# Optimization experiments

Hardware: AMD Instinct MI355X
Metric: run time of the kernel (lower is better)

The kernel has to match this reference:

```python
import jax, jax.numpy as jnp
import numpy as np

N_NODES = 20000
N_EDGES = 320000
N_GRAPHS = 64
SEQ = 20
SCALAR = 16
EMB = 32
HID = 128
HEADS = 4
IN_DIM = SCALAR + 5 * EMB  # 176
NEG_SLOPE = 0.2


def masked_mean_embed(table, idx):
    # table: [V, EMB], idx: [N, L] with 0 = padding
    emb = table[idx]                                  # [N, L, EMB]
    mask = (idx != 0).astype(emb.dtype)[..., None]    # [N, L, 1]
    return (emb * mask).sum(axis=1) / (mask.sum(axis=1) + 1e-9)


def gat_conv(x, src, dst, W, att_src, att_dst, bias, heads, out_ch):
    # PyG GATConv (add_self_loops already applied to src/dst), concat heads.
    N = x.shape[0]
    xw = (x @ W).reshape(N, heads, out_ch)            # [N, H, C]
    a_src = (xw * att_src).sum(-1)                    # [N, H]
    a_dst = (xw * att_dst).sum(-1)                    # [N, H]
    e = jax.nn.leaky_relu(a_src[src] + a_dst[dst], NEG_SLOPE)  # [E, H]
    e_max = jax.ops.segment_max(e, dst, num_segments=N)
    e_max = jnp.where(jnp.isfinite(e_max), e_max, 0.0)
    ex = jnp.exp(e - e_max[dst])                      # [E, H]
    denom = jax.ops.segment_sum(ex, dst, num_segments=N)
    alpha = ex / (denom[dst] + 1e-16)                 # [E, H]
    msg = xw[src] * alpha[:, :, None]                 # [E, H, C]
    out = jax.ops.segment_sum(msg, dst, num_segments=N)
    return out.reshape(N, heads * out_ch) + bias


def setup_inputs() -> dict:
    key = jax.random.key(0)
    ks = jax.random.split(key, 24)
    s = 0.05
    inp = {
        "x_scalar": jax.random.normal(ks[0], (N_NODES, SCALAR), jnp.float32),
        "x_opcode": jax.random.randint(ks[1], (N_NODES, SEQ), 0, 256),
        "x_source": jax.random.randint(ks[2], (N_NODES, SEQ), 0, 512),
        "x_sink": jax.random.randint(ks[3], (N_NODES, SEQ), 0, 512),
        "x_string_manip": jax.random.randint(ks[4], (N_NODES, SEQ), 0, 128),
        "x_payload": jax.random.randint(ks[5], (N_NODES, SEQ), 0, 1024),
        "edge_index": jax.random.randint(ks[6], (2, N_EDGES), 0, N_NODES),
        "batch": jnp.sort(jax.random.randint(ks[7], (N_NODES,), 0, N_GRAPHS)),
        # embedding tables (row 0 = padding; masked out anyway)
        "emb_opcode": jax.random.normal(ks[8], (256, EMB)) * s,
        "emb_source": jax.random.normal(ks[9], (512, EMB)) * s,
        "emb_sink": jax.random.normal(ks[10], (512, EMB)) * s,
        "emb_string": jax.random.normal(ks[11], (128, EMB)) * s,
        "emb_payload": jax.random.normal(ks[12], (1024, EMB)) * s,
        "ln_gamma": jnp.ones((IN_DIM,), jnp.float32),
        "ln_beta": jnp.zeros((IN_DIM,), jnp.float32),
        "W1": jax.random.normal(ks[13], (IN_DIM, HEADS * HID)) * s,
        "att_src1": jax.random.normal(ks[14], (HEADS, HID)) * s,
        "att_dst1": jax.random.normal(ks[15], (HEADS, HID)) * s,
        "b1": jnp.zeros((HEADS * HID,), jnp.float32),
        "W2": jax.random.normal(ks[16], (HEADS * HID, HID)) * s,
        "att_src2": jax.random.normal(ks[17], (1, HID)) * s,
        "att_dst2": jax.random.normal(ks[18], (1, HID)) * s,
        "b2": jnp.zeros((HID,), jnp.float32),
        "cls_w1": jax.random.normal(ks[19], (HID, HID // 2)) * s,
        "cls_b1": jnp.zeros((HID // 2,), jnp.float32),
        "cls_w2": jax.random.normal(ks[20], (HID // 2, 2)) * s,
        "cls_b2": jnp.zeros((2,), jnp.float32),
    }
    return inp


def reference(x_scalar, x_opcode, x_source, x_sink, x_string_manip, x_payload,
              edge_index, batch,
              emb_opcode, emb_source, emb_sink, emb_string, emb_payload,
              ln_gamma, ln_beta,
              W1, att_src1, att_dst1, b1,
              W2, att_src2, att_dst2, b2,
              cls_w1, cls_b1, cls_w2, cls_b2):
    feats = jnp.concatenate([
        x_scalar,
        masked_mean_embed(emb_opcode, x_opcode),
        masked_mean_embed(emb_source, x_source),
        masked_mean_embed(emb_sink, x_sink),
        masked_mean_embed(emb_string, x_string_manip),
        masked_mean_embed(emb_payload, x_payload),
    ], axis=1)  # [N, 176]
    mu = feats.mean(-1, keepdims=True)
    var = ((feats - mu) ** 2).mean(-1, keepdims=True)
    h = (feats - mu) / jnp.sqrt(var + 1e-5) * ln_gamma + ln_beta

    # add self loops (PyG GATConv default)
    loops = jnp.arange(N_NODES, dtype=edge_index.dtype)
    src = jnp.concatenate([edge_index[0], loops])
    dst = jnp.concatenate([edge_index[1], loops])

    x = jax.nn.elu(gat_conv(h, src, dst, W1, att_src1, att_dst1, b1, HEADS, HID))
    x = jax.nn.elu(gat_conv(x, src, dst, W2, att_src2, att_dst2, b2, 1, HID))

    pooled = jax.ops.segment_max(x, batch, num_segments=N_GRAPHS)  # [G, HID]
    hcls = jax.nn.relu(pooled @ cls_w1 + cls_b1)
    return hcls @ cls_w2 + cls_b2  # [G, 2]
```

## Files before the change

### kernel.cpp

```cpp
#include <hip/hip_runtime.h>
#include <hip/hip_bf16.h>
#include <math.h>

#define N_NODES 20000
#define N_EDGES 320000
#define N_GRAPHS 64
#define SEQ 20
#define SCALAR 16
#define EMB 32
#define HID 128
#define IN_DIM 176
#define TOT_EDGES (N_EDGES + N_NODES)
#define CHUNK_SMALL 10000
#define POOL_SLICES 32

typedef _Float16 half8v __attribute__((ext_vector_type(8)));
typedef float f32x4 __attribute__((ext_vector_type(4)));
#define LO_SCALE 2048.0f
#define LO_INV (1.0f / 2048.0f)

#define PB2_ELEMS (16 * 8 * 64 * 8)
#define PB1_ELEMS (4 * 6 * 8 * 64 * 8)

#define SETUP_BLOCKS 124
#define COUNT_BLOCKS ((TOT_EDGES + 255) / 256)
#define NB4 ((N_NODES + 3) / 4)

__device__ inline float readlane_f(float v, int l) {
  return __uint_as_float(__builtin_amdgcn_readlane(__float_as_uint(v), l));
}
__device__ inline int readlane_i(int v, int l) {
  return __builtin_amdgcn_readlane(v, l);
}
__device__ inline float leaky(float e) { return e >= 0.f ? e : 0.2f * e; }
__device__ inline float elu(float v) { return v > 0.f ? v : expf(v) - 1.f; }

__global__ __launch_bounds__(256) void setup_count_kernel(
    const float* __restrict__ W1, const float* __restrict__ att_s1,
    const float* __restrict__ att_d1, const float* __restrict__ W2,
    const int* __restrict__ edge_index, const int* __restrict__ batch,
    float* __restrict__ was4, float* __restrict__ wad4,
    _Float16* __restrict__ PB1h, _Float16* __restrict__ PB1l,
    _Float16* __restrict__ PB2h, _Float16* __restrict__ PB2l,
    int* __restrict__ cnt, int* __restrict__ gstarts) {
  int b = blockIdx.x;
  if (b < 44) {
    int lane = threadIdx.x & 63;
    int k = b * 4 + (threadIdx.x >> 6);
    if (k >= IN_DIM) return;
    const float* wrow = W1 + (size_t)k * 512;
    float s[4], d[4];
#pragma unroll
    for (int hh = 0; hh < 4; ++hh) {
      float w0 = wrow[hh * 128 + lane], w1 = wrow[hh * 128 + 64 + lane];
      float a0 = att_s1[hh * 128 + lane], a1 = att_s1[hh * 128 + 64 + lane];
      float c0 = att_d1[hh * 128 + lane], c1 = att_d1[hh * 128 + 64 + lane];
      s[hh] = w0 * a0 + w1 * a1;
      d[hh] = w0 * c0 + w1 * c1;
    }
    for (int off = 1; off < 64; off <<= 1) {
#pragma unroll
      for (int hh = 0; hh < 4; ++hh) {
        s[hh] += __shfl_xor(s[hh], off);
        d[hh] += __shfl_xor(d[hh], off);
      }
    }
    if (lane == 0) {
      *(float4*)&was4[k * 4] = make_float4(s[0], s[1], s[2], s[3]);
      *(float4*)&wad4[k * 4] = make_float4(d[0], d[1], d[2], d[3]);
    }
  } else if (b < 92) {
    int t = (b - 44) * 256 + threadIdx.x;
    int lane = t & 63, wi = t >> 6;
    int r = lane & 15, g = lane >> 4;
    int ntile = wi & 7, rem = wi >> 3;
    int ks = rem % 6, hh = rem / 6;
    int col = hh * 128 + ntile * 16 + r;
    size_t o = ((size_t)wi * 64 + lane) * 8;
#pragma unroll
// ... 10 lines not shown
    int r = lane & 15, g = lane >> 4;
    int ks = wi >> 3, ntile = wi & 7;
    int col = ntile * 16 + r;
    size_t o = ((size_t)wi * 64 + lane) * 8;
#pragma unroll
    for (int j = 0; j < 8; ++j) {
      int k = ks * 32 + g * 8 + j;
      float v = W2[(size_t)k * 128 + col];
      _Float16 h = (_Float16)v;
      PB2h[o + j] = h;
      PB2l[o + j] = (_Float16)((v - (float)h) * LO_SCALE);
    }
  } else if (b < SETUP_BLOCKS + COUNT_BLOCKS) {
    int i = (b - SETUP_BLOCKS) * 256 + threadIdx.x;
    if (i < N_EDGES) {
      atomicAdd(&cnt[edge_index[N_EDGES + i]], 1);
    } else if (i < TOT_EDGES) {
      atomicAdd(&cnt[i - N_EDGES], 1);
    }
  } else {
    int t = threadIdx.x;
    if (t > N_GRAPHS) return;
    int lo = 0, hi = N_NODES;
    while (lo < hi) {
      int mid = (lo + hi) >> 1;
      if (batch[mid] < t) lo = mid + 1; else hi = mid;
    }
    gstarts[t] = lo;
  }
}

__global__ __launch_bounds__(1024) void prefix_kernel(const int* __restrict__ cnt,
                                                      int* __restrict__ indptr,
                                                      int n, int total) {
  __shared__ int ss[1024];
  int t = threadIdx.x;
  int per = (n + 1023) / 1024;
  int beg = t * per, end = min(beg + per, n);
  int s = 0;
  for (int i = beg; i < end; ++i) s += cnt[i];
  ss[t] = s;
  __syncthreads();
  for (int off = 1; off < 1024; off <<= 1) {
    int v = (t >= off) ? ss[t - off] : 0;
    __syncthreads();
    ss[t] += v;
    __syncthreads();
  }
  int run = ss[t] - s;
  for (int i = beg; i < end; ++i) { indptr[i] = run; run += cnt[i]; }
  if (t == 0) indptr[n] = total;
}

__global__ __launch_bounds__(256) void scatter_feats_kernel(
    const int* __restrict__ edge_index, const int* __restrict__ indptr,
    int* __restrict__ cursor, int* __restrict__ srcs,
    const float* __restrict__ xs,
    const int* __restrict__ i0, const int* __restrict__ i1,
    const int* __restrict__ i2, const int* __restrict__ i3,
    const int* __restrict__ i4,
    const float* __restrict__ t0, const float* __restrict__ t1,
    const float* __restrict__ t2, const float* __restrict__ t3,
    const float* __restrict__ t4,
    const float* __restrict__ gamma, const float* __restrict__ beta,
    const float* __restrict__ was4, const float* __restrict__ wad4,
    float* __restrict__ hout, float* __restrict__ a_s,
    float* __restrict__ a_d) {
  int b = blockIdx.x;
  if (b < COUNT_BLOCKS) {
    int i = b * 256 + threadIdx.x;
    int s, d;
    if (i < N_EDGES) { s = edge_index[i]; d = edge_index[N_EDGES + i]; }
    else if (i < TOT_EDGES) { s = i - N_EDGES; d = s; }
    else return;
    int pos = indptr[d] + atomicAdd(&cursor[d], 1);
    srcs[pos] = s;
    return;
  }
  int lane = threadIdx.x & 63;
  int w = threadIdx.x >> 6;
  int n = (b - COUNT_BLOCKS) * 4 + w;
  if (n >= N_NODES) return;
  __shared__ int sidx[4][100];
  {
    int j = lane;
    int tab = j / 20, l = j - tab * 20;
    const int* ip = tab == 0 ? i0 : tab == 1 ? i1 : tab == 2 ? i2 : i3;
    sidx[w][j] = ip[n * SEQ + l];
    if (lane < 36) {
      int j2 = 64 + lane;
      int tab2 = j2 / 20, l2 = j2 - tab2 * 20;
      const int* ip2 = tab2 == 3 ? i3 : i4;
      sidx[w][j2] = ip2[n * SEQ + l2];
    }
  }
  bool l48 = lane < 48;
  float f0, f1, f2 = 0.f;
  if (lane < SCALAR) {
    f0 = xs[n * SCALAR + lane];
  } else {
    int tt = lane - SCALAR, tab = tt >> 5, d = tt & 31;
    const float* tp = tab == 0 ? t0 : t1;
    float sum = 0.f, cnt = 0.f;
#pragma unroll
    for (int l = 0; l < SEQ; ++l) {
      int id = sidx[w][tab * 20 + l];
      if (id != 0) { sum += tp[id * EMB + d]; cnt += 1.f; }
    }
    f0 = sum / (cnt + 1e-9f);
  }
  {
    int tt = 48 + lane, tab = tt >> 5, d = tt & 31;
    const float* tp = tab == 1 ? t1 : tab == 2 ? t2 : t3;
    float sum = 0.f, cnt = 0.f;
#pragma unroll
    for (int l = 0; l < SEQ; ++l) {
      int id = sidx[w][tab * 20 + l];
      if (id != 0) { sum += tp[id * EMB + d]; cnt += 1.f; }
    }
    f1 = sum / (cnt + 1e-9f);
  }
  if (l48) {
    int tt = 112 + lane, tab = tt >> 5, d = tt & 31;
    const float* tp = tab == 3 ? t3 : t4;
    float sum = 0.f, cnt = 0.f;
#pragma unroll
    for (int l = 0; l < SEQ; ++l) {
      int id = sidx[w][tab * 20 + l];
      if (id != 0) { sum += tp[id * EMB + d]; cnt += 1.f; }
    }
    f2 = sum / (cnt + 1e-9f);
  }
  float s = f0 + f1 + f2;
  for (int off = 1; off < 64; off <<= 1) s += __shfl_xor(s, off);
  float mu = s / (float)IN_DIM;
  float v = (f0 - mu) * (f0 - mu) + (f1 - mu) * (f1 - mu) +
            (l48 ? (f2 - mu) * (f2 - mu) : 0.f);
  for (int off = 1; off < 64; off <<= 1) v += __shfl_xor(v, off);
  float rstd = 1.0f / sqrtf(v / (float)IN_DIM + 1e-5f);
  float hv0 = (f0 - mu) * rstd * gamma[lane] + beta[lane];
  float hv1 = (f1 - mu) * rstd * gamma[64 + lane] + beta[64 + lane];
  float hv2 = l48 ? (f2 - mu) * rstd * gamma[128 + lane] + beta[128 + lane] : 0.f;
  float* hr = hout + (size_t)n * IN_DIM;
  hr[lane] = hv0;
  hr[64 + lane] = hv1;
  if (l48) hr[128 + lane] = hv2;

  const float4* wsv = (const float4*)was4;
  const float4* wdv = (const float4*)wad4;
  float4 wsa = wsv[lane], wsb = wsv[64 + lane];
  float4 wsc = l48 ? wsv[128 + lane] : make_float4(0.f, 0.f, 0.f, 0.f);
  float4 wda = wdv[lane], wdb = wdv[64 + lane];
  float4 wdc = l48 ? wdv[128 + lane] : make_float4(0.f, 0.f, 0.f, 0.f);
  float ps0 = hv0 * wsa.x + hv1 * wsb.x + hv2 * wsc.x;
  float ps1 = hv0 * wsa.y + hv1 * wsb.y + hv2 * wsc.y;
  float ps2 = hv0 * wsa.z + hv1 * wsb.z + hv2 * wsc.z;
  float ps3 = hv0 * wsa.w + hv1 * wsb.w + hv2 * wsc.w;
  float pd0 = hv0 * wda.x + hv1 * wdb.x + hv2 * wdc.x;
  float pd1 = hv0 * wda.y + hv1 * wdb.y + hv2 * wdc.y;
  float pd2 = hv0 * wda.z + hv1 * wdb.z + hv2 * wdc.z;
  float pd3 = hv0 * wda.w + hv1 * wdb.w + hv2 * wdc.w;
  for (int off = 1; off < 64; off <<= 1) {
    ps0 += __shfl_xor(ps0, off); ps1 += __shfl_xor(ps1, off);
    ps2 += __shfl_xor(ps2, off); ps3 += __shfl_xor(ps3, off);
    pd0 += __shfl_xor(pd0, off); pd1 += __shfl_xor(pd1, off);
    pd2 += __shfl_xor(pd2, off); pd3 += __shfl_xor(pd3, off);
  }
  if (lane == 0) {
    *(float4*)&a_s[n * 4] = make_float4(ps0, ps1, ps2, ps3);
    *(float4*)&a_d[n * 4] = make_float4(pd0, pd1, pd2, pd3);
  }
}

__global__ __launch_bounds__(256) void agg1h_kernel(
    const float* __restrict__ h, const float* __restrict__ a_src,
    const float* __restrict__ a_dst, const int* __restrict__ indptr,
    const int* __restrict__ srcs, float* __restrict__ aggh,
    int n0, int nM) {
  int lane = threadIdx.x & 63;
  int ln = blockIdx.x * 4 + (threadIdx.x >> 6);
  if (ln >= nM) return;
  int n = n0 + ln;
  int beg = indptr[n], end = indptr[n + 1];
  int deg = end - beg;
  float4 ad = *(const float4*)&a_dst[n * 4];
  bool l48 = lane < 48;
  float acc[4][3] = {};

  auto body = [&](int s, float al0, float al1, float al2, float al3) {
    const float* r = h + (size_t)s * IN_DIM;
    float v0 = r[lane];
    float v1 = r[64 + lane];
    float v2 = l48 ? r[128 + lane] : 0.f;
    acc[0][0] += al0 * v0; acc[0][1] += al0 * v1; acc[0][2] += al0 * v2;
    acc[1][0] += al1 * v0; acc[1][1] += al1 * v1; acc[1][2] += al1 * v2;
    acc[2][0] += al2 * v0; acc[2][1] += al2 * v1; acc[2][2] += al2 * v2;
    acc[3][0] += al3 * v0; acc[3][1] += al3 * v1; acc[3][2] += al3 * v2;
  };

  if (deg <= 64) {
    int j = beg + lane;
    int s = 0;
    float e0 = -INFINITY, e1 = -INFINITY, e2 = -INFINITY, e3 = -INFINITY;
    if (j < end) {
      s = srcs[j];
      float4 as = *(const float4*)&a_src[s * 4];
      e0 = leaky(as.x + ad.x); e1 = leaky(as.y + ad.y);
      e2 = leaky(as.z + ad.z); e3 = leaky(as.w + ad.w);
    }
    float m0 = e0, m1 = e1, m2 = e2, m3 = e3;
    for (int off = 1; off < 64; off <<= 1) {
      m0 = fmaxf(m0, __shfl_xor(m0, off)); m1 = fmaxf(m1, __shfl_xor(m1, off));
      m2 = fmaxf(m2, __shfl_xor(m2, off)); m3 = fmaxf(m3, __shfl_xor(m3, off));
    }
    float x0 = (j < end) ? expf(e0 - m0) : 0.f;
    float x1 = (j < end) ? expf(e1 - m1) : 0.f;
    float x2 = (j < end) ? expf(e2 - m2) : 0.f;
    float x3 = (j < end) ? expf(e3 - m3) : 0.f;
    float d0 = x0, d1 = x1, d2 = x2, d3 = x3;
    for (int off = 1; off < 64; off <<= 1) {
      d0 += __shfl_xor(d0, off); d1 += __shfl_xor(d1, off);
      d2 += __shfl_xor(d2, off); d3 += __shfl_xor(d3, off);
    }
    float al0 = x0 / (d0 + 1e-16f), al1 = x1 / (d1 + 1e-16f);
    float al2 = x2 / (d2 + 1e-16f), al3 = x3 / (d3 + 1e-16f);
    int jj = 0;
    for (; jj + 2 <= deg; jj += 2) {
      int sa = readlane_i(s, jj), sb = readlane_i(s, jj + 1);
      float a0 = readlane_f(al0, jj), a1 = readlane_f(al1, jj);
      float a2 = readlane_f(al2, jj), a3 = readlane_f(al3, jj);
      float b0 = readlane_f(al0, jj + 1), b1 = readlane_f(al1, jj + 1);
      float b2 = readlane_f(al2, jj + 1), b3 = readlane_f(al3, jj + 1);
      body(sa, a0, a1, a2, a3);
// ... 14 lines not shown
        m0 = fmaxf(m0, leaky(as.x + ad.x)); m1 = fmaxf(m1, leaky(as.y + ad.y));
        m2 = fmaxf(m2, leaky(as.z + ad.z)); m3 = fmaxf(m3, leaky(as.w + ad.w));
      }
    }
    for (int off = 1; off < 64; off <<= 1) {
      m0 = fmaxf(m0, __shfl_xor(m0, off)); m1 = fmaxf(m1, __shfl_xor(m1, off));
      m2 = fmaxf(m2, __shfl_xor(m2, off)); m3 = fmaxf(m3, __shfl_xor(m3, off));
    }
    float d0 = 0.f, d1 = 0.f, d2 = 0.f, d3 = 0.f;
    for (int j0 = beg; j0 < end; j0 += 64) {
      int j = j0 + lane;
      if (j < end) {
        int s = srcs[j];
        float4 as = *(const float4*)&a_src[s * 4];
        d0 += expf(leaky(as.x + ad.x) - m0); d1 += expf(leaky(as.y + ad.y) - m1);
        d2 += expf(leaky(as.z + ad.z) - m2); d3 += expf(leaky(as.w + ad.w) - m3);
      }
    }
    for (int off = 1; off < 64; off <<= 1) {
      d0 += __shfl_xor(d0, off); d1 += __shfl_xor(d1, off);
      d2 += __shfl_xor(d2, off); d3 += __shfl_xor(d3, off);
    }
    float r0 = 1.f / (d0 + 1e-16f), r1 = 1.f / (d1 + 1e-16f);
    float r2 = 1.f / (d2 + 1e-16f), r3 = 1.f / (d3 + 1e-16f);
    for (int j0 = beg; j0 < end; j0 += 64) {
      int jn = min(64, end - j0);
      int j = j0 + lane;
      int s = 0;
      float al0 = 0.f, al1 = 0.f, al2 = 0.f, al3 = 0.f;
      if (j < end) {
        s = srcs[j];
        float4 as = *(const float4*)&a_src[s * 4];
        al0 = expf(leaky(as.x + ad.x) - m0) * r0;
        al1 = expf(leaky(as.y + ad.y) - m1) * r1;
        al2 = expf(leaky(as.z + ad.z) - m2) * r2;
        al3 = expf(leaky(as.w + ad.w) - m3) * r3;
      }
      for (int jj = 0; jj < jn; ++jj) {
        body(readlane_i(s, jj), readlane_f(al0, jj), readlane_f(al1, jj),
             readlane_f(al2, jj), readlane_f(al3, jj));
      }
    }
  }

  size_t base = (size_t)ln * (4 * IN_DIM);
#pragma unroll
  for (int hh = 0; hh < 4; ++hh) {
    aggh[base + hh * IN_DIM + lane] = acc[hh][0];
    aggh[base + hh * IN_DIM + 64 + lane] = acc[hh][1];
    if (l48) aggh[base + hh * IN_DIM + 128 + lane] = acc[hh][2];
  }
}

__global__ __launch_bounds__(256) void gemm_head_mfma_kernel(
    const float* __restrict__ aggh, const half8v* __restrict__ PBh,
    const half8v* __restrict__ PBl, const float* __restrict__ b1,
    float* __restrict__ out1, int M, int n0) {
  int lane = threadIdx.x & 63;
  int wid = (blockIdx.x * 256 + threadIdx.x) >> 6;
  int colhalf = wid & 1;
  int hh = (wid >> 1) & 3;
  int rg = wid >> 3;
  int rows0 = rg * 16;
  if (rows0 >= M) return;
  int r = lane & 15, g = lane >> 4;
  f32x4 acc[4] = {};
  f32x4 accm[4] = {};
  const float* a0 = aggh + ((size_t)(rows0 + r) * 4 + hh) * IN_DIM;
#pragma unroll 2
  for (int ks = 0; ks < 6; ++ks) {
    int kg = ks * 32 + g * 8;
    int koff = (kg + 8 <= IN_DIM) ? kg : 0;
    const float* ap = a0 + koff;
    float av[8];
    *(float4*)&av[0] = *(const float4*)(ap);
    *(float4*)&av[4] = *(const float4*)(ap + 4);
    half8v ah, al;
#pragma unroll
    for (int j = 0; j < 8; ++j) {
      _Float16 hv = (_Float16)av[j];
      ah[j] = hv;
      al[j] = (_Float16)((av[j] - (float)hv) * LO_SCALE);
    }
    const half8v* bh = PBh + (size_t)(((hh * 6 + ks) * 8 + colhalf * 4) * 64) + lane;
    const half8v* bl = PBl + (size_t)(((hh * 6 + ks) * 8 + colhalf * 4) * 64) + lane;
#pragma unroll
    for (int nt = 0; nt < 4; ++nt) {
      half8v bhv = bh[nt * 64], blv = bl[nt * 64];
      accm[nt] = __builtin_amdgcn_mfma_f32_16x16x32_f16(al, bhv, accm[nt], 0, 0, 0);
      accm[nt] = __builtin_amdgcn_mfma_f32_16x16x32_f16(ah, blv, accm[nt], 0, 0, 0);
      acc[nt]  = __builtin_amdgcn_mfma_f32_16x16x32_f16(ah, bhv, acc[nt], 0, 0, 0);
    }
  }
#pragma unroll
  for (int nt = 0; nt < 4; ++nt) {
    int col = hh * 128 + colhalf * 64 + nt * 16 + r;
    float bb = b1[col];
#pragma unroll
    for (int i = 0; i < 4; ++i) {
      int row = rows0 + g * 4 + i;
      if (row < M)
        out1[(size_t)(n0 + row) * 512 + col] =
            elu(acc[nt][i] + accm[nt][i] * LO_INV + bb);
    }
  }
}

__global__ __launch_bounds__(256) void gemm2att_mfma_kernel(
    const float* __restrict__ A, const half8v* __restrict__ PBh,
    const half8v* __restrict__ PBl, const float* __restrict__ att_s,
    const float* __restrict__ att_d, float* __restrict__ C,
    float* __restrict__ a_s, float* __restrict__ a_d, int M) {
  int lane = threadIdx.x & 63;
  int wid = (blockIdx.x * 256 + threadIdx.x) >> 6;
  int colq = wid & 3;
  int rg = wid >> 2;
  int row0 = rg * 16;
  if (row0 >= M) return;
  int r = lane & 15, g = lane >> 4;
  const float* arow = A + (size_t)(row0 + r) * 512 + g * 8;
  f32x4 acc[2] = {};
  f32x4 accm[2] = {};
#pragma unroll 2
  for (int ks = 0; ks < 16; ++ks) {
    float av[8];
    *(float4*)&av[0] = *(const float4*)(arow + ks * 32);
    *(float4*)&av[4] = *(const float4*)(arow + ks * 32 + 4);
    half8v ah, al;
#pragma unroll
    for (int j = 0; j < 8; ++j) {
      _Float16 hv = (_Float16)av[j];
      ah[j] = hv;
      al[j] = (_Float16)((av[j] - (float)hv) * LO_SCALE);
    }
    const half8v* bh = PBh + (size_t)((ks * 8 + colq * 2) * 64) + lane;
    const half8v* bl = PBl + (size_t)((ks * 8 + colq * 2) * 64) + lane;
#pragma unroll
    for (int nt = 0; nt < 2; ++nt) {
      half8v bhv = bh[nt * 64], blv = bl[nt * 64];
      accm[nt] = __builtin_amdgcn_mfma_f32_16x16x32_f16(al, bhv, accm[nt], 0, 0, 0);
      accm[nt] = __builtin_amdgcn_mfma_f32_16x16x32_f16(ah, blv, accm[nt], 0, 0, 0);
      acc[nt]  = __builtin_amdgcn_mfma_f32_16x16x32_f16(ah, bhv, acc[nt], 0, 0, 0);
    }
  }
  float ps[4] = {0.f, 0.f, 0.f, 0.f}, pd[4] = {0.f, 0.f, 0.f, 0.f};
#pragma unroll
  for (int nt = 0; nt < 2; ++nt) {
    int col = colq * 32 + nt * 16 + r;
    float as_ = att_s[col], ad_ = att_d[col];
#pragma unroll
    for (int i = 0; i < 4; ++i) {
      float v = acc[nt][i] + accm[nt][i] * LO_INV;
      int row = row0 + g * 4 + i;
      C[(size_t)row * 128 + col] = v;
      ps[i] += v * as_;
      pd[i] += v * ad_;
    }
  }
#pragma unroll
  for (int i = 0; i < 4; ++i) {
    for (int off = 1; off < 16; off <<= 1) {
      ps[i] += __shfl_xor(ps[i], off);
      pd[i] += __shfl_xor(pd[i], off);
    }
  }
  if (r == 0) {
#pragma unroll
    for (int i = 0; i < 4; ++i) {
      atomicAdd(&a_s[row0 + g * 4 + i], ps[i]);
      atomicAdd(&a_d[row0 + g * 4 + i], pd[i]);
    }
  }
}

__global__ __launch_bounds__(256) void agg2_kernel(
    const float* __restrict__ xw, const float* __restrict__ a_src,
    const float* __restrict__ a_dst, const int* __restrict__ indptr,
    const int* __restrict__ srcs, const float* __restrict__ bias,
    float* __restrict__ out) {
  int lane = threadIdx.x & 63;
  int n = blockIdx.x * 4 + (threadIdx.x >> 6);
  if (n >= N_NODES) return;
  int beg = indptr[n], end = indptr[n + 1];
  int deg = end - beg;
  float adn = a_dst[n];
  int half = lane >> 5, l32 = lane & 31;
  float4 acc = make_float4(0.f, 0.f, 0.f, 0.f);

  auto pairs = [&](int s, float al, int jn) {
    int jj = 0;
    for (; jj + 2 <= jn; jj += 2) {
      int sa = readlane_i(s, jj), sb = readlane_i(s, jj + 1);
      float aa = readlane_f(al, jj), ab = readlane_f(al, jj + 1);
      int sh = half ? sb : sa;
      float ahx = half ? ab : aa;
      float4 v = *(const float4*)&xw[(size_t)sh * HID + l32 * 4];
      acc.x += ahx * v.x; acc.y += ahx * v.y; acc.z += ahx * v.z; acc.w += ahx * v.w;
    }
    if (jj < jn) {
      int sa = readlane_i(s, jj);
      float ahx = half ? 0.f : readlane_f(al, jj);
      float4 v = *(const float4*)&xw[(size_t)sa * HID + l32 * 4];
      acc.x += ahx * v.x; acc.y += ahx * v.y; acc.z += ahx * v.z; acc.w += ahx * v.w;
    }
  };

  if (deg <= 64) {
    int j = beg + lane;
    int s = 0;
    float e = -INFINITY;
    if (j < end) { s = srcs[j]; e = leaky(a_src[s] + adn); }
    float m = e;
    for (int off = 1; off < 64; off <<= 1) m = fmaxf(m, __shfl_xor(m, off));
    float x = (j < end) ? expf(e - m) : 0.f;
    float d = x;
    for (int off = 1; off < 64; off <<= 1) d += __shfl_xor(d, off);
    float al = x / (d + 1e-16f);
    pairs(s, al, deg);
  } else {
    float m = -INFINITY;
    for (int j0 = beg; j0 < end; j0 += 64) {
      int j = j0 + lane;
      if (j < end) m = fmaxf(m, leaky(a_src[srcs[j]] + adn));
    }
    for (int off = 1; off < 64; off <<= 1) m = fmaxf(m, __shfl_xor(m, off));
// ... 55 lines not shown
                                                  const float* __restrict__ w1,
                                                  const float* __restrict__ b1,
                                                  const float* __restrict__ w2,
                                                  const float* __restrict__ b2,
                                                  float* __restrict__ out) {
  int g = blockIdx.x, t = threadIdx.x;
  __shared__ float sp[HID], sh1[HID / 2];
  sp[t] = pooled[g * HID + t];
  __syncthreads();
  if (t < HID / 2) {
    float s = b1[t];
    for (int k = 0; k < HID; ++k) s += sp[k] * w1[k * (HID / 2) + t];
    sh1[t] = fmaxf(s, 0.f);
  }
  __syncthreads();
  if (t < 2) {
    float o = b2[t];
    for (int k = 0; k < HID / 2; ++k) o += sh1[k] * w2[k * 2 + t];
    out[g * 2 + t] = o;
  }
}

extern "C" void kernel_launch(void* const* d_in, const int* in_sizes, int n_in,
                              void* d_out, int out_size, void* d_ws, size_t ws_size,
                              hipStream_t stream) {
  const float* x_scalar = (const float*)d_in[0];
  const int* x_opcode   = (const int*)d_in[1];
  const int* x_source   = (const int*)d_in[2];
  const int* x_sink     = (const int*)d_in[3];
  const int* x_string   = (const int*)d_in[4];
  const int* x_payload  = (const int*)d_in[5];
  const int* edge_index = (const int*)d_in[6];
  const int* batch      = (const int*)d_in[7];
  const float* emb_opcode = (const float*)d_in[8];
  const float* emb_source = (const float*)d_in[9];
  const float* emb_sink   = (const float*)d_in[10];
  const float* emb_string = (const float*)d_in[11];
  const float* emb_payload= (const float*)d_in[12];
  const float* ln_gamma = (const float*)d_in[13];
  const float* ln_beta  = (const float*)d_in[14];
  const float* W1       = (const float*)d_in[15];
  const float* att_src1 = (const float*)d_in[16];
  const float* att_dst1 = (const float*)d_in[17];
  const float* b1       = (const float*)d_in[18];
  const float* W2       = (const float*)d_in[19];
  const float* att_src2 = (const float*)d_in[20];
  const float* att_dst2 = (const float*)d_in[21];
  const float* b2       = (const float*)d_in[22];
  const float* cls_w1   = (const float*)d_in[23];
  const float* cls_b1   = (const float*)d_in[24];
  const float* cls_w2   = (const float*)d_in[25];
  const float* cls_b2   = (const float*)d_in[26];

  auto total_bytes = [&](int chunk) -> size_t {
    size_t f = (size_t)N_NODES * IN_DIM + (size_t)chunk * 4 * IN_DIM +
               (size_t)N_NODES * 512 + (size_t)N_NODES * HID +
               N_NODES * 4 * 2 + N_NODES * 2 + IN_DIM * 4 * 2 + N_GRAPHS * HID;
    size_t ii = (N_NODES + 1) + N_NODES * 2 + TOT_EDGES + (N_GRAPHS + 1);
    size_t f16b = (size_t)2 * (PB2_ELEMS + PB1_ELEMS) * sizeof(_Float16) + 32;
    size_t poolb = (size_t)N_GRAPHS * POOL_SLICES * HID * 4 + 32;
    return f * 4 + ii * 4 + f16b + poolb + 256;
  };
  int chunk = (ws_size >= total_bytes(N_NODES)) ? N_NODES : CHUNK_SMALL;

  float* h      = (float*)d_ws;
  float* aggh   = h + (size_t)N_NODES * IN_DIM;
  float* out1   = aggh + (size_t)chunk * 4 * IN_DIM;
  float* out2   = out1 + (size_t)N_NODES * 512;
  float* a1s    = out2 + (size_t)N_NODES * HID;
  float* a1d    = a1s + N_NODES * 4;
  float* was4   = a1d + N_NODES * 4;
  float* wad4   = was4 + IN_DIM * 4;
  float* pooled = wad4 + IN_DIM * 4;
  int* indptr = (int*)(pooled + N_GRAPHS * HID);
  int* cnt    = indptr + (N_NODES + 1);
  int* cursor = cnt + N_NODES;
  float* a2s  = (float*)(cursor + N_NODES);
  float* a2d  = a2s + N_NODES;
  int* srcs   = (int*)(a2d + N_NODES);
  int* gstarts= srcs + TOT_EDGES;
  uintptr_t pal = ((uintptr_t)(gstarts + N_GRAPHS + 1) + 15) & ~(uintptr_t)15;
  _Float16* PB2h = (_Float16*)pal;
  _Float16* PB2l = PB2h + PB2_ELEMS;
  _Float16* PB1h = PB2l + PB2_ELEMS;
  _Float16* PB1l = PB1h + PB1_ELEMS;
  uintptr_t ppal = ((uintptr_t)(PB1l + PB1_ELEMS) + 15) & ~(uintptr_t)15;
  float* pool_part = (float*)ppal;
  float* xw2  = h;

  hipMemsetAsync(cnt, 0, 4 * N_NODES * sizeof(int), stream);

  setup_count_kernel<<<SETUP_BLOCKS + COUNT_BLOCKS + 1, 256, 0, stream>>>(
      W1, att_src1, att_dst1, W2, edge_index, batch,
      was4, wad4, PB1h, PB1l, PB2h, PB2l, cnt, gstarts);

  prefix_kernel<<<1, 1024, 0, stream>>>(cnt, indptr, N_NODES, TOT_EDGES);

  scatter_feats_kernel<<<COUNT_BLOCKS + NB4, 256, 0, stream>>>(
      edge_index, indptr, cursor, srcs,
      x_scalar, x_opcode, x_source, x_sink, x_string, x_payload,
      emb_opcode, emb_source, emb_sink, emb_string, emb_payload,
      ln_gamma, ln_beta, was4, wad4, h, a1s, a1d);

  for (int n0 = 0; n0 < N_NODES; n0 += chunk) {
    int nM = min(chunk, N_NODES - n0);
    agg1h_kernel<<<(nM + 3) / 4, 256, 0, stream>>>(h, a1s, a1d, indptr, srcs, aggh, n0, nM);
    int rgs = (nM + 15) / 16;
    gemm_head_mfma_kernel<<<rgs * 2, 256, 0, stream>>>(
        aggh, (const half8v*)PB1h, (const half8v*)PB1l, b1, out1, nM, n0);
  }

  gemm2att_mfma_kernel<<<(N_NODES + 15) / 16, 256, 0, stream>>>(
      out1, (const half8v*)PB2h, (const half8v*)PB2l, att_src2, att_dst2,
      xw2, a2s, a2d, N_NODES);

  agg2_kernel<<<NB4, 256, 0, stream>>>(xw2, a2s, a2d, indptr, srcs, b2, out2);

  pool_part_kernel<<<dim3(N_GRAPHS, POOL_SLICES), HID, 0, stream>>>(out2, gstarts, pool_part);
  pool_reduce_kernel<<<N_GRAPHS, HID, 0, stream>>>(pool_part, pooled);
  cls_kernel<<<N_GRAPHS, HID, 0, stream>>>(pooled, cls_w1, cls_b1, cls_w2, cls_b2, (float*)d_out);
}
```

Before: 368.0 us.

## Software-pipeline layer-1 aggregation, head GEMM and layer-2 GEMM across node chunks

Splits the nodes into four chunks and launches a fused mid kernel per stage whose blocks run agg1h on chunk s, the head GEMM on chunk s-1 and the layer-2 GEMM plus attention on chunk s-2. The aim is to overlap the memory-bound gather with the MFMA GEMMs and fill the GPU across stages. To avoid a write conflict, xw2 gets its own buffer instead of aliasing h, which needs more workspace, and the feature blocks are moved ahead of the edge scatter blocks in the grid. The cost is more launches (six stages) and a heterogeneous block mix that may cause imbalance.

```diff
diff --git a/kernel.cpp b/kernel.cpp
--- a/kernel.cpp
+++ b/kernel.cpp
@@ -25,6 +25,13 @@
 #define SETUP_BLOCKS 124
 #define COUNT_BLOCKS ((TOT_EDGES + 255) / 256)
 #define NB4 ((N_NODES + 3) / 4)
+
+#define NCHUNK 4
+#define CH (N_NODES / NCHUNK)
+#define MB_AGG ((CH + 3) / 4)
+#define MB_GEMM (((CH + 15) / 16) * 2)
+#define MB_Q ((CH + 15) / 16)
+#define MID_BLOCKS (MB_AGG + MB_GEMM + MB_Q)
 
 __device__ inline float readlane_f(float v, int l) {
   return __uint_as_float(__builtin_amdgcn_readlane(__float_as_uint(v), l));
@@ -141,7 +148,7 @@
   if (t == 0) indptr[n] = total;
 }
 
-__global__ __launch_bounds__(256) void scatter_feats_kernel(
+__global__ __launch_bounds__(256) void feats_scatter_kernel(
     const int* __restrict__ edge_index, const int* __restrict__ indptr,
     int* __restrict__ cursor, int* __restrict__ srcs,
     const float* __restrict__ xs,
@@ -156,8 +163,8 @@
     float* __restrict__ hout, float* __restrict__ a_s,
     float* __restrict__ a_d) {
   int b = blockIdx.x;
-  if (b < COUNT_BLOCKS) {
-    int i = b * 256 + threadIdx.x;
+  if (b >= NB4) {
+    int i = (b - NB4) * 256 + threadIdx.x;
     int s, d;
     if (i < N_EDGES) { s = edge_index[i]; d = edge_index[N_EDGES + i]; }
     else if (i < TOT_EDGES) { s = i - N_EDGES; d = s; }
@@ -168,7 +175,7 @@
   }
   int lane = threadIdx.x & 63;
   int w = threadIdx.x >> 6;
-  int n = (b - COUNT_BLOCKS) * 4 + w;
+  int n = b * 4 + w;
   if (n >= N_NODES) return;
   __shared__ int sidx[4][100];
   {
@@ -261,13 +268,13 @@
   }
 }
 
-__global__ __launch_bounds__(256) void agg1h_kernel(
-    const float* __restrict__ h, const float* __restrict__ a_src,
+__device__ __forceinline__ void agg1h_body(
+    int lb, const float* __restrict__ h, const float* __restrict__ a_src,
     const float* __restrict__ a_dst, const int* __restrict__ indptr,
-    const int* __restrict__ srcs, float* __restrict__ aggh,
+    const int* __restrict__ srcs, float* __restrict__ aggh ,
     int n0, int nM) {
   int lane = threadIdx.x & 63;
-  int ln = blockIdx.x * 4 + (threadIdx.x >> 6);
+  int ln = lb * 4 + (threadIdx.x >> 6);
   if (ln >= nM) return;
   int n = n0 + ln;
   int beg = indptr[n], end = indptr[n + 1];
@@ -388,17 +395,17 @@
   }
 }
 
-__global__ __launch_bounds__(256) void gemm_head_mfma_kernel(
-    const float* __restrict__ aggh, const half8v* __restrict__ PBh,
-    const half8v* __restrict__ PBl, const float* __restrict__ b1,
-    float* __restrict__ out1, int M, int n0) {
+__device__ __forceinline__ void gemm_head_body(
+    int lb, const float* __restrict__ aggh ,
+    const half8v* __restrict__ PBh, const half8v* __restrict__ PBl,
+    const float* __restrict__ b1, float* __restrict__ out1, int n0, int nM) {
   int lane = threadIdx.x & 63;
-  int wid = (blockIdx.x * 256 + threadIdx.x) >> 6;
+  int wid = (lb * 256 + threadIdx.x) >> 6;
   int colhalf = wid & 1;
   int hh = (wid >> 1) & 3;
   int rg = wid >> 3;
   int rows0 = rg * 16;
-  if (rows0 >= M) return;
+  if (rows0 >= nM) return;
   int r = lane & 15, g = lane >> 4;
   f32x4 acc[4] = {};
   f32x4 accm[4] = {};
@@ -435,26 +442,27 @@
 #pragma unroll
     for (int i = 0; i < 4; ++i) {
       int row = rows0 + g * 4 + i;
-      if (row < M)
+      if (row < nM)
         out1[(size_t)(n0 + row) * 512 + col] =
             elu(acc[nt][i] + accm[nt][i] * LO_INV + bb);
     }
   }
 }
 
-__global__ __launch_bounds__(256) void gemm2att_mfma_kernel(
-    const float* __restrict__ A, const half8v* __restrict__ PBh,
-    const half8v* __restrict__ PBl, const float* __restrict__ att_s,
-    const float* __restrict__ att_d, float* __restrict__ C,
-    float* __restrict__ a_s, float* __restrict__ a_d, int M) {
+__device__ __forceinline__ void gemm2att_body(
+    int lb, const float* __restrict__ A ,
+    const half8v* __restrict__ PBh, const half8v* __restrict__ PBl,
+    const float* __restrict__ att_s, const float* __restrict__ att_d,
+    float* __restrict__ C, float* __restrict__ a_s, float* __restrict__ a_d,
+    int n0, int nM) {
   int lane = threadIdx.x & 63;
-  int wid = (blockIdx.x * 256 + threadIdx.x) >> 6;
+  int wid = (lb * 256 + threadIdx.x) >> 6;
   int colq = wid & 3;
   int rg = wid >> 2;
   int row0 = rg * 16;
-  if (row0 >= M) return;
+  if (row0 >= nM) return;
   int r = lane & 15, g = lane >> 4;
-  const float* arow = A + (size_t)(row0 + r) * 512 + g * 8;
+  const float* arow = A + (size_t)(n0 + row0 + r) * 512 + g * 8;
   f32x4 acc[2] = {};
   f32x4 accm[2] = {};
 #pragma unroll 2
@@ -488,7 +496,7 @@
     for (int i = 0; i < 4; ++i) {
       float v = acc[nt][i] + accm[nt][i] * LO_INV;
       int row = row0 + g * 4 + i;
-      C[(size_t)row * 128 + col] = v;
+      if (row < nM) C[(size_t)(n0 + row) * 128 + col] = v;
       ps[i] += v * as_;
       pd[i] += v * ad_;
     }
@@ -503,10 +511,60 @@
   if (r == 0) {
 #pragma unroll
     for (int i = 0; i < 4; ++i) {
-      atomicAdd(&a_s[row0 + g * 4 + i], ps[i]);
-      atomicAdd(&a_d[row0 + g * 4 + i], pd[i]);
-    }
-  }
+      int row = row0 + g * 4 + i;
+      if (row < nM) {
+        atomicAdd(&a_s[n0 + row], ps[i]);
+        atomicAdd(&a_d[n0 + row], pd[i]);
+      }
+    }
+  }
+}
+
+__global__ __launch_bounds__(256) void mid_kernel(
+    const float* __restrict__ h, const float* __restrict__ a1s,
+    const float* __restrict__ a1d, const int* __restrict__ indptr,
+    const int* __restrict__ srcs, float* __restrict__ agghA,
+    const float* __restrict__ agghG,
+    const half8v* __restrict__ PB1h, const half8v* __restrict__ PB1l,
+    const float* __restrict__ b1, float* __restrict__ out1,
+    const half8v* __restrict__ PB2h, const half8v* __restrict__ PB2l,
+    const float* __restrict__ att_s2, const float* __restrict__ att_d2,
+    float* __restrict__ xw2, float* __restrict__ a2s, float* __restrict__ a2d,
+    int na0, int ng0, int nq0) {
+  int b = blockIdx.x;
+  if (b < MB_AGG) {
+    if (na0 < 0) return;
+    agg1h_body(b, h, a1s, a1d, indptr, srcs, agghA, na0,
+               min(CH, N_NODES - na0));
+  } else if (b < MB_AGG + MB_GEMM) {
+    if (ng0 < 0) return;
+    gemm_head_body(b - MB_AGG, agghG, PB1h, PB1l, b1, out1, ng0,
+                   min(CH, N_NODES - ng0));
+  } else {
+    if (nq0 < 0) return;
+    gemm2att_body(b - MB_AGG - MB_GEMM, out1, PB2h, PB2l, att_s2, att_d2,
+                  xw2, a2s, a2d, nq0, min(CH, N_NODES - nq0));
+  }
+}
+
+__global__ __launch_bounds__(256) void agg1h_kernel(
+    const float* __restrict__ h, const float* __restrict__ a_src,
+    const float* __restrict__ a_dst, const int* __restrict__ indptr,
+    const int* __restrict__ srcs, float* __restrict__ aggh, int n0, int nM) {
+  agg1h_body(blockIdx.x, h, a_src, a_dst, indptr, srcs, aggh, n0, nM);
+}
+__global__ __launch_bounds__(256) void gemm_head_kernel(
+    const float* __restrict__ aggh, const half8v* __restrict__ PBh,
+    const half8v* __restrict__ PBl, const float* __restrict__ b1,
+    float* __restrict__ out1, int n0, int nM) {
+  gemm_head_body(blockIdx.x, aggh, PBh, PBl, b1, out1, n0, nM);
+}
+__global__ __launch_bounds__(256) void gemm2att_kernel(
+    const float* __restrict__ A, const half8v* __restrict__ PBh,
+    const half8v* __restrict__ PBl, const float* __restrict__ att_s,
+    const float* __restrict__ att_d, float* __restrict__ C,
+    float* __restrict__ a_s, float* __restrict__ a_d, int n0, int nM) {
+  gemm2att_body(blockIdx.x, A, PBh, PBl, att_s, att_d, C, a_s, a_d, n0, nM);
 }
 
 __global__ __launch_bounds__(256) void agg2_kernel(
@@ -668,16 +726,18 @@
   const float* cls_w2   = (const float*)d_in[25];
   const float* cls_b2   = (const float*)d_in[26];
 
-  auto total_bytes = [&](int chunk) -> size_t {
+  auto total_bytes = [&](int chunk, bool sep_xw2) -> size_t {
     size_t f = (size_t)N_NODES * IN_DIM + (size_t)chunk * 4 * IN_DIM +
                (size_t)N_NODES * 512 + (size_t)N_NODES * HID +
-               N_NODES * 4 * 2 + N_NODES * 2 + IN_DIM * 4 * 2 + N_GRAPHS * HID;
+               N_NODES * 4 * 2 + N_NODES * 2 + IN_DIM * 4 * 2 + N_GRAPHS * HID +
+               (sep_xw2 ? (size_t)N_NODES * HID : 0);
     size_t ii = (N_NODES + 1) + N_NODES * 2 + TOT_EDGES + (N_GRAPHS + 1);
     size_t f16b = (size_t)2 * (PB2_ELEMS + PB1_ELEMS) * sizeof(_Float16) + 32;
     size_t poolb = (size_t)N_GRAPHS * POOL_SLICES * HID * 4 + 32;
     return f * 4 + ii * 4 + f16b + poolb + 256;
   };
-  int chunk = (ws_size >= total_bytes(N_NODES)) ? N_NODES : CHUNK_SMALL;
+  bool pipelined = ws_size >= total_bytes(N_NODES, true);
+  int chunk = pipelined ? N_NODES : CHUNK_SMALL;
 
   float* h      = (float*)d_ws;
   float* aggh   = h + (size_t)N_NODES * IN_DIM;
@@ -688,7 +748,9 @@
   float* was4   = a1d + N_NODES * 4;
   float* wad4   = was4 + IN_DIM * 4;
   float* pooled = wad4 + IN_DIM * 4;
-  int* indptr = (int*)(pooled + N_GRAPHS * HID);
+  float* xw2base= pooled + N_GRAPHS * HID;
+  float* after  = pipelined ? (xw2base + (size_t)N_NODES * HID) : xw2base;
+  int* indptr = (int*)after;
   int* cnt    = indptr + (N_NODES + 1);
   int* cursor = cnt + N_NODES;
   float* a2s  = (float*)(cursor + N_NODES);
@@ -702,7 +764,7 @@
   _Float16* PB1l = PB1h + PB1_ELEMS;
   uintptr_t ppal = ((uintptr_t)(PB1l + PB1_ELEMS) + 15) & ~(uintptr_t)15;
   float* pool_part = (float*)ppal;
-  float* xw2  = h;
+  float* xw2 = pipelined ? xw2base : h;
 
   hipMemsetAsync(cnt, 0, 4 * N_NODES * sizeof(int), stream);
 
@@ -712,23 +774,37 @@
 
   prefix_kernel<<<1, 1024, 0, stream>>>(cnt, indptr, N_NODES, TOT_EDGES);
 
-  scatter_feats_kernel<<<COUNT_BLOCKS + NB4, 256, 0, stream>>>(
+  feats_scatter_kernel<<<NB4 + COUNT_BLOCKS, 256, 0, stream>>>(
       edge_index, indptr, cursor, srcs,
       x_scalar, x_opcode, x_source, x_sink, x_string, x_payload,
       emb_opcode, emb_source, emb_sink, emb_string, emb_payload,
       ln_gamma, ln_beta, was4, wad4, h, a1s, a1d);
 
-  for (int n0 = 0; n0 < N_NODES; n0 += chunk) {
-    int nM = min(chunk, N_NODES - n0);
-    agg1h_kernel<<<(nM + 3) / 4, 256, 0, stream>>>(h, a1s, a1d, indptr, srcs, aggh, n0, nM);
-    int rgs = (nM + 15) / 16;
-    gemm_head_mfma_kernel<<<rgs * 2, 256, 0, stream>>>(
-        aggh, (const half8v*)PB1h, (const half8v*)PB1l, b1, out1, nM, n0);
-  }
-
-  gemm2att_mfma_kernel<<<(N_NODES + 15) / 16, 256, 0, stream>>>(
-      out1, (const half8v*)PB2h, (const half8v*)PB2l, att_src2, att_dst2,
-      xw2, a2s, a2d, N_NODES);
+  if (pipelined) {
+    for (int s = 0; s < NCHUNK + 2; ++s) {
+      int na0 = (s < NCHUNK) ? s * CH : -1;
+      int ng0 = (s >= 1 && s <= NCHUNK) ? (s - 1) * CH : -1;
+      int nq0 = (s >= 2 && s <= NCHUNK + 1) ? (s - 2) * CH : -1;
+      float* agghA = aggh + (na0 > 0 ? (size_t)na0 * 4 * IN_DIM : 0);
+      const float* agghG = aggh + (ng0 > 0 ? (size_t)ng0 * 4 * IN_DIM : 0);
+      mid_kernel<<<MID_BLOCKS, 256, 0, stream>>>(
+          h, a1s, a1d, indptr, srcs, agghA, agghG,
+          (const half8v*)PB1h, (const half8v*)PB1l, b1, out1,
+          (const half8v*)PB2h, (const half8v*)PB2l, att_src2, att_dst2,
+          xw2, a2s, a2d, na0, ng0, nq0);
+    }
+  } else {
+    for (int n0 = 0; n0 < N_NODES; n0 += chunk) {
+      int nM = min(chunk, N_NODES - n0);
+      agg1h_kernel<<<(nM + 3) / 4, 256, 0, stream>>>(h, a1s, a1d, indptr, srcs,
+                                                     aggh, n0, nM);
+      gemm_head_kernel<<<((nM + 15) / 16) * 2, 256, 0, stream>>>(
+          aggh, (const half8v*)PB1h, (const half8v*)PB1l, b1, out1, n0, nM);
+    }
+    gemm2att_kernel<<<(N_NODES + 15) / 16, 256, 0, stream>>>(
+        out1, (const half8v*)PB2h, (const half8v*)PB2l, att_src2, att_dst2,
+        xw2, a2s, a2d, 0, N_NODES);
+  }
 
   agg2_kernel<<<NB4, 256, 0, stream>>>(xw2, a2s, a2d, indptr, srcs, b2, out2);
 
```

Measured after the change: 407.3 us. +10.7%, slower.

## Fuse layer-1 head GEMM and layer-2 GEMM via shared-memory tile

Applied to the files above, without the earlier changes.

Merges the per-head layer-1 GEMM (with bias and ELU) and the layer-2 GEMM with attention projections into one 512-thread kernel. The 16x512 layer-1 output tile stays in LDS instead of being written to a global N x 512 buffer and read back. It also swaps the block order in the scatter/feature kernel so the feature blocks come first and the edge-scatter blocks follow. The cost is a block barrier, about 33KB of LDS per block, and fewer, larger blocks, which may lower occupancy.

```diff
diff --git a/kernel.cpp b/kernel.cpp
--- a/kernel.cpp
+++ b/kernel.cpp
@@ -141,7 +141,7 @@
   if (t == 0) indptr[n] = total;
 }
 
-__global__ __launch_bounds__(256) void scatter_feats_kernel(
+__global__ __launch_bounds__(256) void feats_scatter_kernel(
     const int* __restrict__ edge_index, const int* __restrict__ indptr,
     int* __restrict__ cursor, int* __restrict__ srcs,
     const float* __restrict__ xs,
@@ -156,8 +156,8 @@
     float* __restrict__ hout, float* __restrict__ a_s,
     float* __restrict__ a_d) {
   int b = blockIdx.x;
-  if (b < COUNT_BLOCKS) {
-    int i = b * 256 + threadIdx.x;
+  if (b >= NB4) {
+    int i = (b - NB4) * 256 + threadIdx.x;
     int s, d;
     if (i < N_EDGES) { s = edge_index[i]; d = edge_index[N_EDGES + i]; }
     else if (i < TOT_EDGES) { s = i - N_EDGES; d = s; }
@@ -168,7 +168,7 @@
   }
   int lane = threadIdx.x & 63;
   int w = threadIdx.x >> 6;
-  int n = (b - COUNT_BLOCKS) * 4 + w;
+  int n = b * 4 + w;
   if (n >= N_NODES) return;
   __shared__ int sidx[4][100];
   {
@@ -388,123 +388,112 @@
   }
 }
 
-__global__ __launch_bounds__(256) void gemm_head_mfma_kernel(
-    const float* __restrict__ aggh, const half8v* __restrict__ PBh,
-    const half8v* __restrict__ PBl, const float* __restrict__ b1,
-    float* __restrict__ out1, int M, int n0) {
+__global__ __launch_bounds__(512) void gemm_fused_kernel(
+    const float* __restrict__ aggh, const half8v* __restrict__ PB1h,
+    const half8v* __restrict__ PB1l, const float* __restrict__ b1,
+    const half8v* __restrict__ PB2h, const half8v* __restrict__ PB2l,
+    const float* __restrict__ att_s, const float* __restrict__ att_d,
+    float* __restrict__ xw2, float* __restrict__ a_s, float* __restrict__ a_d,
+    int n0, int nM) {
+  __shared__ float s1[16][516];
   int lane = threadIdx.x & 63;
-  int wid = (blockIdx.x * 256 + threadIdx.x) >> 6;
-  int colhalf = wid & 1;
-  int hh = (wid >> 1) & 3;
-  int rg = wid >> 3;
-  int rows0 = rg * 16;
-  if (rows0 >= M) return;
+  int w = threadIdx.x >> 6;
+  int rows0 = blockIdx.x * 16;
+  if (rows0 >= nM) return;
   int r = lane & 15, g = lane >> 4;
-  f32x4 acc[4] = {};
-  f32x4 accm[4] = {};
-  const float* a0 = aggh + ((size_t)(rows0 + r) * 4 + hh) * IN_DIM;
+
+  {
+    int hh = w >> 1, colhalf = w & 1;
+    f32x4 acc[4] = {};
+    f32x4 accm[4] = {};
+    const float* a0 = aggh + ((size_t)(rows0 + r) * 4 + hh) * IN_DIM;
 #pragma unroll 2
-  for (int ks = 0; ks < 6; ++ks) {
-    int kg = ks * 32 + g * 8;
-    int koff = (kg + 8 <= IN_DIM) ? kg : 0;
-    const float* ap = a0 + koff;
-    float av[8];
-    *(float4*)&av[0] = *(const float4*)(ap);
-    *(float4*)&av[4] = *(const float4*)(ap + 4);
-    half8v ah, al;
-#pragma unroll
-    for (int j = 0; j < 8; ++j) {
-      _Float16 hv = (_Float16)av[j];
-      ah[j] = hv;
-      al[j] = (_Float16)((av[j] - (float)hv) * LO_SCALE);
-    }
-    const half8v* bh = PBh + (size_t)(((hh * 6 + ks) * 8 + colhalf * 4) * 64) + lane;
-    const half8v* bl = PBl + (size_t)(((hh * 6 + ks) * 8 + colhalf * 4) * 64) + lane;
+    for (int ks = 0; ks < 6; ++ks) {
+      int kg = ks * 32 + g * 8;
+      int koff = (kg + 8 <= IN_DIM) ? kg : 0;
+      const float* ap = a0 + koff;
+      float av[8];
+      *(float4*)&av[0] = *(const float4*)(ap);
+      *(float4*)&av[4] = *(const float4*)(ap + 4);
+      half8v ah, al;
+#pragma unroll
+      for (int j = 0; j < 8; ++j) {
+        _Float16 hv = (_Float16)av[j];
+        ah[j] = hv;
+        al[j] = (_Float16)((av[j] - (float)hv) * LO_SCALE);
+      }
+      const half8v* bh = PB1h + (size_t)(((hh * 6 + ks) * 8 + colhalf * 4) * 64) + lane;
+      const half8v* bl = PB1l + (size_t)(((hh * 6 + ks) * 8 + colhalf * 4) * 64) + lane;
+#pragma unroll
+      for (int nt = 0; nt < 4; ++nt) {
+        half8v bhv = bh[nt * 64], blv = bl[nt * 64];
+        accm[nt] = __builtin_amdgcn_mfma_f32_16x16x32_f16(al, bhv, accm[nt], 0, 0, 0);
+        accm[nt] = __builtin_amdgcn_mfma_f32_16x16x32_f16(ah, blv, accm[nt], 0, 0, 0);
+        acc[nt]  = __builtin_amdgcn_mfma_f32_16x16x32_f16(ah, bhv, acc[nt], 0, 0, 0);
+      }
+    }
 #pragma unroll
     for (int nt = 0; nt < 4; ++nt) {
-      half8v bhv = bh[nt * 64], blv = bl[nt * 64];
-      accm[nt] = __builtin_amdgcn_mfma_f32_16x16x32_f16(al, bhv, accm[nt], 0, 0, 0);
-      accm[nt] = __builtin_amdgcn_mfma_f32_16x16x32_f16(ah, blv, accm[nt], 0, 0, 0);
-      acc[nt]  = __builtin_amdgcn_mfma_f32_16x16x32_f16(ah, bhv, acc[nt], 0, 0, 0);
-    }
-  }
-#pragma unroll
-  for (int nt = 0; nt < 4; ++nt) {
-    int col = hh * 128 + colhalf * 64 + nt * 16 + r;
-    float bb = b1[col];
+      int col = hh * 128 + colhalf * 64 + nt * 16 + r;
+      float bb = b1[col];
+#pragma unroll
+      for (int i = 0; i < 4; ++i) {
+        int row = g * 4 + i;
+        if (rows0 + row < nM)
+          s1[row][col] = elu(acc[nt][i] + accm[nt][i] * LO_INV + bb);
+      }
+    }
+  }
+  __syncthreads();
+
+  {
+    f32x4 qacc = {};
+    f32x4 qaccm = {};
+#pragma unroll 2
+    for (int ks = 0; ks < 16; ++ks) {
+      float av[8];
+      *(float4*)&av[0] = *(const float4*)&s1[r][ks * 32 + g * 8];
+      *(float4*)&av[4] = *(const float4*)&s1[r][ks * 32 + g * 8 + 4];
+      half8v ah, al;
+#pragma unroll
+      for (int j = 0; j < 8; ++j) {
+        _Float16 hv = (_Float16)av[j];
+        ah[j] = hv;
+        al[j] = (_Float16)((av[j] - (float)hv) * LO_SCALE);
+      }
+      half8v bhv = PB2h[(size_t)((ks * 8 + w) * 64) + lane];
+      half8v blv = PB2l[(size_t)((ks * 8 + w) * 64) + lane];
+      qaccm = __builtin_amdgcn_mfma_f32_16x16x32_f16(al, bhv, qaccm, 0, 0, 0);
+      qaccm = __builtin_amdgcn_mfma_f32_16x16x32_f16(ah, blv, qaccm, 0, 0, 0);
+      qacc  = __builtin_amdgcn_mfma_f32_16x16x32_f16(ah, bhv, qacc, 0, 0, 0);
+    }
+    int col = w * 16 + r;
+    float as_ = att_s[col], ad_ = att_d[col];
+    float ps[4], pd[4];
 #pragma unroll
     for (int i = 0; i < 4; ++i) {
+      float v = qacc[i] + qaccm[i] * LO_INV;
       int row = rows0 + g * 4 + i;
-      if (row < M)
-        out1[(size_t)(n0 + row) * 512 + col] =
-            elu(acc[nt][i] + accm[nt][i] * LO_INV + bb);
-    }
-  }
-}
-
-__global__ __launch_bounds__(256) void gemm2att_mfma_kernel(
-    const float* __restrict__ A, const half8v* __restrict__ PBh,
-    const half8v* __restrict__ PBl, const float* __restrict__ att_s,
-    const float* __restrict__ att_d, float* __restrict__ C,
-    float* __restrict__ a_s, float* __restrict__ a_d, int M) {
-  int lane = threadIdx.x & 63;
-  int wid = (blockIdx.x * 256 + threadIdx.x) >> 6;
-  int colq = wid & 3;
-  int rg = wid >> 2;
-  int row0 = rg * 16;
-  if (row0 >= M) return;
-  int r = lane & 15, g = lane >> 4;
-  const float* arow = A + (size_t)(row0 + r) * 512 + g * 8;
-  f32x4 acc[2] = {};
-  f32x4 accm[2] = {};
-#pragma unroll 2
-  for (int ks = 0; ks < 16; ++ks) {
-    float av[8];
-    *(float4*)&av[0] = *(const float4*)(arow + ks * 32);
-    *(float4*)&av[4] = *(const float4*)(arow + ks * 32 + 4);
-    half8v ah, al;
-#pragma unroll
-    for (int j = 0; j < 8; ++j) {
-      _Float16 hv = (_Float16)av[j];
-      ah[j] = hv;
-      al[j] = (_Float16)((av[j] - (float)hv) * LO_SCALE);
-    }
-    const half8v* bh = PBh + (size_t)((ks * 8 + colq * 2) * 64) + lane;
-    const half8v* bl = PBl + (size_t)((ks * 8 + colq * 2) * 64) + lane;
-#pragma unroll
-    for (int nt = 0; nt < 2; ++nt) {
-      half8v bhv = bh[nt * 64], blv = bl[nt * 64];
-      accm[nt] = __builtin_amdgcn_mfma_f32_16x16x32_f16(al, bhv, accm[nt], 0, 0, 0);
-      accm[nt] = __builtin_amdgcn_mfma_f32_16x16x32_f16(ah, blv, accm[nt], 0, 0, 0);
-      acc[nt]  = __builtin_amdgcn_mfma_f32_16x16x32_f16(ah, bhv, acc[nt], 0, 0, 0);
-    }
-  }
-  float ps[4] = {0.f, 0.f, 0.f, 0.f}, pd[4] = {0.f, 0.f, 0.f, 0.f};
-#pragma unroll
-  for (int nt = 0; nt < 2; ++nt) {
-    int col = colq * 32 + nt * 16 + r;
-    float as_ = att_s[col], ad_ = att_d[col];
+      if (row < nM) xw2[(size_t)(n0 + row) * 128 + col] = v;
+      ps[i] = v * as_;
+      pd[i] = v * ad_;
+    }
 #pragma unroll
     for (int i = 0; i < 4; ++i) {
-      float v = acc[nt][i] + accm[nt][i] * LO_INV;
-      int row = row0 + g * 4 + i;
-      C[(size_t)row * 128 + col] = v;
-      ps[i] += v * as_;
-      pd[i] += v * ad_;
-    }
-  }
-#pragma unroll
-  for (int i = 0; i < 4; ++i) {
-    for (int off = 1; off < 16; off <<= 1) {
-      ps[i] += __shfl_xor(ps[i], off);
-      pd[i] += __shfl_xor(pd[i], off);
-    }
-  }
-  if (r == 0) {
-#pragma unroll
-    for (int i = 0; i < 4; ++i) {
-      atomicAdd(&a_s[row0 + g * 4 + i], ps[i]);
-      atomicAdd(&a_d[row0 + g * 4 + i], pd[i]);
+      for (int off = 1; off < 16; off <<= 1) {
+        ps[i] += __shfl_xor(ps[i], off);
+        pd[i] += __shfl_xor(pd[i], off);
+      }
+    }
+    if (r == 0) {
+#pragma unroll
+      for (int i = 0; i < 4; ++i) {
+        int row = rows0 + g * 4 + i;
+        if (row < nM) {
+          atomicAdd(&a_s[n0 + row], ps[i]);
+          atomicAdd(&a_d[n0 + row], pd[i]);
+        }
+      }
     }
   }
 }
@@ -670,7 +659,7 @@
 
   auto total_bytes = [&](int chunk) -> size_t {
     size_t f = (size_t)N_NODES * IN_DIM + (size_t)chunk * 4 * IN_DIM +
-               (size_t)N_NODES * 512 + (size_t)N_NODES * HID +
+               (size_t)N_NODES * HID * 2 +
                N_NODES * 4 * 2 + N_NODES * 2 + IN_DIM * 4 * 2 + N_GRAPHS * HID;
     size_t ii = (N_NODES + 1) + N_NODES * 2 + TOT_EDGES + (N_GRAPHS + 1);
     size_t f16b = (size_t)2 * (PB2_ELEMS + PB1_ELEMS) * sizeof(_Float16) + 32;
@@ -681,8 +670,8 @@
 
   float* h      = (float*)d_ws;
   float* aggh   = h + (size_t)N_NODES * IN_DIM;
-  float* out1   = aggh + (size_t)chunk * 4 * IN_DIM;
-  float* out2   = out1 + (size_t)N_NODES * 512;
+  float* xw2    = aggh + (size_t)chunk * 4 * IN_DIM;
+  float* out2   = xw2 + (size_t)N_NODES * HID;
   float* a1s    = out2 + (size_t)N_NODES * HID;
   float* a1d    = a1s + N_NODES * 4;
   float* was4   = a1d + N_NODES * 4;
@@ -702,7 +691,6 @@
   _Float16* PB1l = PB1h + PB1_ELEMS;
   uintptr_t ppal = ((uintptr_t)(PB1l + PB1_ELEMS) + 15) & ~(uintptr_t)15;
   float* pool_part = (float*)ppal;
-  float* xw2  = h;
 
   hipMemsetAsync(cnt, 0, 4 * N_NODES * sizeof(int), stream);
 
@@ -712,7 +700,7 @@
 
   prefix_kernel<<<1, 1024, 0, stream>>>(cnt, indptr, N_NODES, TOT_EDGES);
 
-  scatter_feats_kernel<<<COUNT_BLOCKS + NB4, 256, 0, stream>>>(
+  feats_scatter_kernel<<<NB4 + COUNT_BLOCKS, 256, 0, stream>>>(
       edge_index, indptr, cursor, srcs,
       x_scalar, x_opcode, x_source, x_sink, x_string, x_payload,
       emb_opcode, emb_source, emb_sink, emb_string, emb_payload,
@@ -720,15 +708,13 @@
 
   for (int n0 = 0; n0 < N_NODES; n0 += chunk) {
     int nM = min(chunk, N_NODES - n0);
-    agg1h_kernel<<<(nM + 3) / 4, 256, 0, stream>>>(h, a1s, a1d, indptr, srcs, aggh, n0, nM);
-    int rgs = (nM + 15) / 16;
-    gemm_head_mfma_kernel<<<rgs * 2, 256, 0, stream>>>(
-        aggh, (const half8v*)PB1h, (const half8v*)PB1l, b1, out1, nM, n0);
-  }
-
-  gemm2att_mfma_kernel<<<(N_NODES + 15) / 16, 256, 0, stream>>>(
-      out1, (const half8v*)PB2h, (const half8v*)PB2l, att_src2, att_dst2,
-      xw2, a2s, a2d, N_NODES);
+    agg1h_kernel<<<(nM + 3) / 4, 256, 0, stream>>>(h, a1s, a1d, indptr, srcs,
+                                                   aggh, n0, nM);
+    gemm_fused_kernel<<<(nM + 15) / 16, 512, 0, stream>>>(
+        aggh, (const half8v*)PB1h, (const half8v*)PB1l, b1,
+        (const half8v*)PB2h, (const half8v*)PB2l, att_src2, att_dst2,
+        xw2, a2s, a2d, n0, nM);
+  }
 
   agg2_kernel<<<NB4, 256, 0, stream>>>(xw2, a2s, a2d, indptr, srcs, b2, out2);
 
```

Result: faster. 355.7 us (-3.3%).
